# Kernel tuning notes

Measured on AMD Instinct MI355X. Metric: run time of the kernel, lower is better.

Reference implementation:

```python
import jax, jax.numpy as jnp
import numpy as np

DECAY = 0.99
EPS = 1e-05


def setup_inputs() -> dict:
    key = jax.random.key(0)
    k1, k2 = jax.random.split(key)
    B, C, H, W = 16, 64, 64, 64
    dim, n_embed = 64, 2048
    x = jax.random.normal(k1, (B, C, H, W), dtype=jnp.float32)
    embed = jax.random.normal(k2, (dim, n_embed), dtype=jnp.float32)
    cluster_size = jnp.zeros((n_embed,), dtype=jnp.float32)
    embed_avg = embed.copy()
    return {"x": x, "embed": embed, "cluster_size": cluster_size, "embed_avg": embed_avg}


def reference(x, embed, cluster_size, embed_avg):
    # x: [B, C, H, W], embed: [dim, n_embed]
    dim, n_embed = embed.shape
    xp = jnp.transpose(x, (0, 2, 3, 1))            # [B, H, W, dim]
    flat = xp.reshape(-1, dim)                     # [N, dim]

    # Pairwise squared distances: ||f||^2 - 2 f.E + ||e||^2  -> [N, n_embed]
    dist = (jnp.sum(flat * flat, axis=1, keepdims=True)
            - 2.0 * (flat @ embed)
            + jnp.sum(embed * embed, axis=0, keepdims=True))
    embed_ind_flat = jnp.argmin(dist, axis=1)      # [N]

    # Gather codes (embed_code)
    quantize = embed.T[embed_ind_flat].reshape(xp.shape)  # [B, H, W, dim]
    embed_ind = embed_ind_flat.reshape(xp.shape[:-1])     # [B, H, W]

    # Training-mode EMA codebook update (functional; buffers returned)
    counts = jax.ops.segment_sum(jnp.ones_like(embed_ind_flat, dtype=flat.dtype),
                                 embed_ind_flat, num_segments=n_embed)      # onehot.sum(0)
    embed_sum = jax.ops.segment_sum(flat, embed_ind_flat,
                                    num_segments=n_embed).T                 # flat.T @ onehot -> [dim, n_embed]
    new_cluster_size = DECAY * cluster_size + (1.0 - DECAY) * counts
    new_embed_avg = DECAY * embed_avg + (1.0 - DECAY) * embed_sum
    n = jnp.sum(new_cluster_size)
    cs = (new_cluster_size + EPS) / (n + n_embed * EPS) * n
    new_embed = new_embed_avg / cs[None, :]

    diff = jnp.mean((jax.lax.stop_gradient(quantize) - xp) ** 2)
    quantize_st = xp + jax.lax.stop_gradient(quantize - xp)
    out = jnp.transpose(quantize_st, (0, 3, 1, 2))  # back to NCHW
    return out, diff, embed_ind, new_embed, new_cluster_size, new_embed_avg
```

## Files before the change

kernel.cpp:

```cpp
#include <hip/hip_runtime.h>
#include <stdint.h>

#define DIM 64
#define NE 2048
#define NROWS 65536
#define HW 4096

#define DECAYF 0.99f
#define OMDF ((float)(1.0 - 0.99))
#define EPSF 1e-5f
#define NEPSF ((float)(2048.0 * 1e-5))

typedef _Float16 f16x8 __attribute__((ext_vector_type(8)));
typedef float f32x4 __attribute__((ext_vector_type(4)));

#define SPLIT_SCALE 1024.0f
#define SPLIT_INV 0.0009765625f

__global__ __launch_bounds__(256) void se_kernel(const float* __restrict__ E,
                                                 float* __restrict__ se) {
  int j = blockIdx.x * 256 + threadIdx.x;
  float s = 0.f;
#pragma unroll
  for (int d = 0; d < DIM; ++d) {
    float v = E[d * NE + j];
    s += v * v;
  }
  se[j] = s;
}

__global__ __launch_bounds__(256) void epack_kernel(const float* __restrict__ E,
                                                    _Float16* __restrict__ Eh,
                                                    _Float16* __restrict__ El) {
  int task = blockIdx.x * 256 + threadIdx.x;
  int l = task & 63;
  int ks = (task >> 6) & 1;
  int t = task >> 7;
  int j = t * 16 + (l & 15);
  int d0 = ks * 32 + ((l >> 4) & 3) * 8;
  _Float16 h8[8], l8[8];
#pragma unroll
  for (int r = 0; r < 8; ++r) {
    float v = E[(d0 + r) * NE + j];
    _Float16 h = (_Float16)v;
    h8[r] = h;
    l8[r] = (_Float16)((v - (float)h) * SPLIT_SCALE);
  }
  *(f16x8*)(Eh + (size_t)task * 8) = *(f16x8*)h8;
  *(f16x8*)(El + (size_t)task * 8) = *(f16x8*)l8;
}

#define MFMA16(A, B, C) __builtin_amdgcn_mfma_f32_16x16x32_f16(A, B, C, 0, 0, 0)

#define COMPUTE_TILE(T, B0, B1, B2, B3, SEJ)                              \
  {                                                                       \
    _Pragma("unroll") for (int rt = 0; rt < 4; ++rt) {                    \
      f32x4 a1 = {0.f, 0.f, 0.f, 0.f};                                    \
      f32x4 a2 = {0.f, 0.f, 0.f, 0.f};                                    \
      a1 = MFMA16(xh[rt][0], B0, a1);                                     \
      a1 = MFMA16(xh[rt][1], B1, a1);                                     \
      a2 = MFMA16(xh[rt][0], B2, a2);                                     \
      a2 = MFMA16(xh[rt][1], B3, a2);                                     \
      a2 = MFMA16(xl[rt][0], B0, a2);                                     \
      a2 = MFMA16(xl[rt][1], B1, a2);                                     \
      _Pragma("unroll") for (int q = 0; q < 4; ++q) {                     \
        float dot = fmaf(a2[q], SPLIT_INV, a1[q]);                        \
        float dist = fmaf(-2.f, dot, SEJ);                                \
        if (dist < bv[rt][q]) { bv[rt][q] = dist; bi[rt][q] = (T)*16 + lc; } \
      }                                                                   \
    }                                                                     \
  }

__global__ __launch_bounds__(256, 1) void argmin_mfma_kernel(
    const float* __restrict__ x, const _Float16* __restrict__ Eh,
    const _Float16* __restrict__ El, const float* __restrict__ se,
    int* __restrict__ ind, float* __restrict__ ind_f) {
  const int tid = threadIdx.x;
  const int lane = tid & 63;
  const int wv = tid >> 6;
  const int R0 = blockIdx.x * 256 + wv * 64;
  const int lg = (lane >> 4) & 3;
  const int lc = lane & 15;

  f16x8 xh[4][2], xl[4][2];
#pragma unroll
  for (int rt = 0; rt < 4; ++rt) {
#pragma unroll
    for (int ks = 0; ks < 2; ++ks) {
      int r_glob = R0 + rt * 16 + lc;
      const float* xr = x + (size_t)(r_glob >> 12) * (DIM * HW) + (r_glob & 4095);
      int d0 = ks * 32 + lg * 8;
      _Float16 h8[8], l8[8];
#pragma unroll
      for (int e = 0; e < 8; ++e) {
        float v = xr[(d0 + e) * HW];
        _Float16 h = (_Float16)v;
        h8[e] = h;
        l8[e] = (_Float16)((v - (float)h) * SPLIT_SCALE);
      }
      xh[rt][ks] = *(f16x8*)h8;
      xl[rt][ks] = *(f16x8*)l8;
    }
  }

  float bv[4][4];
  int bi[4][4];
#pragma unroll
  for (int rt = 0; rt < 4; ++rt)
#pragma unroll
    for (int q = 0; q < 4; ++q) { bv[rt][q] = 3.4e38f; bi[rt][q] = 0; }

  const size_t lo = (size_t)lane * 8;
  f16x8 c0 = *(const f16x8*)(Eh + lo);
  f16x8 c1 = *(const f16x8*)(Eh + 512 + lo);
  f16x8 c2 = *(const f16x8*)(El + lo);
  f16x8 c3 = *(const f16x8*)(El + 512 + lo);
  float seC = se[lc];

  for (int t = 0; t < NE / 16; t += 2) {
    f16x8 n0 = *(const f16x8*)(Eh + (size_t)(t + 1) * 1024 + lo);
    f16x8 n1 = *(const f16x8*)(Eh + (size_t)(t + 1) * 1024 + 512 + lo);
    f16x8 n2 = *(const f16x8*)(El + (size_t)(t + 1) * 1024 + lo);
    f16x8 n3 = *(const f16x8*)(El + (size_t)(t + 1) * 1024 + 512 + lo);
    float seN = se[(t + 1) * 16 + lc];

    COMPUTE_TILE(t, c0, c1, c2, c3, seC);

    if (t + 2 < NE / 16) {
      c0 = *(const f16x8*)(Eh + (size_t)(t + 2) * 1024 + lo);
      c1 = *(const f16x8*)(Eh + (size_t)(t + 2) * 1024 + 512 + lo);
      c2 = *(const f16x8*)(El + (size_t)(t + 2) * 1024 + lo);
      c3 = *(const f16x8*)(El + (size_t)(t + 2) * 1024 + 512 + lo);
      seC = se[(t + 2) * 16 + lc];
    }

    COMPUTE_TILE(t + 1, n0, n1, n2, n3, seN);
  }

#pragma unroll
  for (int rt = 0; rt < 4; ++rt) {
#pragma unroll
    for (int q = 0; q < 4; ++q) {
      float v = bv[rt][q];
      int ix = bi[rt][q];
#pragma unroll
      for (int off = 1; off < 16; off <<= 1) {
        float ov = __shfl_xor(v, off, 64);
        int oi = __shfl_xor(ix, off, 64);
        if (ov < v || (ov == v && oi < ix)) { v = ov; ix = oi; }
      }
      if (lc == 0) {
        int grow = R0 + rt * 16 + lg * 4 + q;
        ind[grow] = ix;
        ind_f[grow] = (float)ix;
      }
    }
  }
}

__global__ __launch_bounds__(256) void esum_fused_kernel(const float* __restrict__ x,
                                                         const float* __restrict__ E,
                                                         const int* __restrict__ ind,
                                                         float* __restrict__ out,
                                                         float* __restrict__ diff_acc,
                                                         float* __restrict__ pesum,
                                                         int* __restrict__ pcnt) {
  const int d = blockIdx.x >> 2;
  const int bg = blockIdx.x & 3;
  __shared__ float h[4][NE];
  __shared__ int cnt[NE];
  const int tid = threadIdx.x;
  const int w = tid >> 6;
  float* hf = &h[0][0];
#pragma unroll
  for (int u = 0; u < 32; ++u) hf[u * 256 + tid] = 0.f;
  if (d == 0) {
#pragma unroll
    for (int u = 0; u < 8; ++u) cnt[u * 256 + tid] = 0;
  }
  __syncthreads();
  const float* Ed = E + d * NE;
  float local = 0.f;
  for (int b = bg * 4; b < bg * 4 + 4; ++b) {
    const int* ib = ind + b * 4096;
    const float* xb = x + ((size_t)b * DIM + d) * 4096;
    float* ob = out + ((size_t)b * DIM + d) * 4096;
#pragma unroll 4
    for (int it = 0; it < 16; ++it) {
      int i = it * 256 + tid;
      int idx = ib[i];
      float xv = xb[i];
      float qv = Ed[idx];
      float dq = qv - xv;
      ob[i] = xv + dq;
      local += dq * dq;
      atomicAdd(&h[w][idx], xv);
      if (d == 0) atomicAdd(&cnt[idx], 1);
    }
  }
#pragma unroll
  for (int off = 32; off > 0; off >>= 1) local += __shfl_down(local, off, 64);
  __shared__ float wsum[4];
  if ((tid & 63) == 0) wsum[tid >> 6] = local;
  __syncthreads();
  if (tid == 0) {
    float s = (wsum[0] + wsum[1]) + (wsum[2] + wsum[3]);
    atomicAdd(diff_acc, s * (1.f / 4194304.f));
  }
  float* pe = pesum + ((size_t)bg * DIM + d) * NE;
#pragma unroll
  for (int u = 0; u < 8; ++u) {
    int j = u * 256 + tid;
    pe[j] = (h[0][j] + h[1][j]) + (h[2][j] + h[3][j]);
  }
  if (d == 0) {
    int* pc = pcnt + bg * NE;
#pragma unroll
    for (int u = 0; u < 8; ++u) {
      int j = u * 256 + tid;
      pc[j] = cnt[j];
    }
  }
}

__global__ __launch_bounds__(1024) void finalize_a4(const float* __restrict__ cs_in,
                                                    const int* __restrict__ pcnt,
                                                    float* __restrict__ ncs_slot,
                                                    float* __restrict__ n_out) {
  const int t = threadIdx.x;
  float local = 0.f;
#pragma unroll
  for (int u = 0; u < 2; ++u) {
    int k = u * 1024 + t;
    int c = (pcnt[k] + pcnt[NE + k]) + (pcnt[2 * NE + k] + pcnt[3 * NE + k]);
    float v = DECAYF * cs_in[k] + OMDF * (float)c;
    ncs_slot[k] = v;
    local += v;
  }
#pragma unroll
  for (int off = 32; off > 0; off >>= 1) local += __shfl_down(local, off, 64);
  __shared__ float red[16];
  if ((t & 63) == 0) red[t >> 6] = local;
  __syncthreads();
  if (t == 0) {
    float s = 0.f;
#pragma unroll
    for (int k = 0; k < 16; ++k) s += red[k];
    *n_out = s;
  }
}

__global__ __launch_bounds__(256) void finalize_b4(const float* __restrict__ ea_in,
                                                   const float* __restrict__ pesum,
                                                   const float* __restrict__ ncs_slot,
                                                   const float* __restrict__ n_out,
                                                   float* __restrict__ nea_slot,
                                                   float* __restrict__ ne_slot) {
  const int k = blockIdx.x * 256 + threadIdx.x;
  const float n = *n_out;
  const size_t P = (size_t)DIM * NE;
  float es = (pesum[k] + pesum[P + k]) + (pesum[2 * P + k] + pesum[3 * P + k]);
  float nea = DECAYF * ea_in[k] + OMDF * es;
  nea_slot[k] = nea;
  float ncs = ncs_slot[k & (NE - 1)];
  float cs = (ncs + EPSF) / (n + NEPSF) * n;
  ne_slot[k] = nea / cs;
}

#define BRF 128
#define TCF 128
#define NTF (NE / TCF)
__global__ __launch_bounds__(256, 2) void argmin_lds_kernel(const float* __restrict__ x,
                                                            const float* __restrict__ E,
                                                            const float* __restrict__ se,
                                                            int* __restrict__ ind,
                                                            float* __restrict__ ind_f) {
  __shared__ float Xs[DIM][BRF];
  __shared__ float Es[DIM][TCF];
  const int tid = threadIdx.x;
  const int rg = tid >> 4;
  const int cg = tid & 15;
  const int B0 = blockIdx.x * BRF;
  const float* xb = x + (size_t)(B0 >> 12) * (DIM * HW) + (B0 & 4095);
  float* Xf = &Xs[0][0];
#pragma unroll
  for (int k = 0; k < 8; ++k) {
    int i = k * 1024 + tid * 4;
    *(float4*)(Xf + i) = *(const float4*)(xb + (i >> 7) * HW + (i & 127));
  }
  float bv[8];
  int bi[8];
#pragma unroll
  for (int i2 = 0; i2 < 8; ++i2) { bv[i2] = 3.4e38f; bi[i2] = 0; }
  float* Ef = &Es[0][0];
  for (int t = 0; t < NTF; ++t) {
    __syncthreads();
#pragma unroll
    for (int k = 0; k < 8; ++k) {
      int i = k * 1024 + tid * 4;
      *(float4*)(Ef + i) = *(const float4*)(E + (i >> 7) * NE + t * TCF + (i & 127));
    }
    __syncthreads();
    float acc[8][8];
#pragma unroll
    for (int i2 = 0; i2 < 8; ++i2)
#pragma unroll
      for (int j = 0; j < 8; ++j) acc[i2][j] = 0.f;
#pragma unroll 8
    for (int d = 0; d < DIM; ++d) {
      float4 xa = *(const float4*)&Xs[d][rg * 8];
      float4 xc = *(const float4*)&Xs[d][rg * 8 + 4];
      float4 ea = *(const float4*)&Es[d][cg * 4];
      float4 ec = *(const float4*)&Es[d][cg * 4 + 64];
      float xr[8] = {xa.x, xa.y, xa.z, xa.w, xc.x, xc.y, xc.z, xc.w};
      float er[8] = {ea.x, ea.y, ea.z, ea.w, ec.x, ec.y, ec.z, ec.w};
#pragma unroll
      for (int i2 = 0; i2 < 8; ++i2)
#pragma unroll
        for (int j = 0; j < 8; ++j) acc[i2][j] = fmaf(xr[i2], er[j], acc[i2][j]);
    }
    float4 s0 = *(const float4*)(se + t * TCF + cg * 4);
    float4 s1 = *(const float4*)(se + t * TCF + cg * 4 + 64);
    float sv[8] = {s0.x, s0.y, s0.z, s0.w, s1.x, s1.y, s1.z, s1.w};
#pragma unroll
    for (int i2 = 0; i2 < 8; ++i2) {
#pragma unroll
      for (int j = 0; j < 8; ++j) {
        float dist = fmaf(-2.f, acc[i2][j], sv[j]);
        if (dist < bv[i2]) {
          bv[i2] = dist;
          bi[i2] = t * TCF + (j >> 2) * 64 + cg * 4 + (j & 3);
        }
      }
    }
  }
#pragma unroll
  for (int i2 = 0; i2 < 8; ++i2) {
    float v = bv[i2];
    int ix = bi[i2];
#pragma unroll
    for (int off = 1; off < 16; off <<= 1) {
      float ov = __shfl_xor(v, off, 64);
      int oi = __shfl_xor(ix, off, 64);
      if (ov < v || (ov == v && oi < ix)) { v = ov; ix = oi; }
    }
    bv[i2] = v;
    bi[i2] = ix;
  }
  if (cg == 0) {
#pragma unroll
    for (int i2 = 0; i2 < 8; ++i2) {
      int grow = B0 + rg * 8 + i2;
      ind[grow] = bi[i2];
      ind_f[grow] = (float)bi[i2];
    }
  }
}

__global__ __launch_bounds__(256) void outdiff_kernel(const float* __restrict__ x,
                                                      const float* __restrict__ E,
                                                      const int* __restrict__ ind,
                                                      float* __restrict__ out,
                                                      float* __restrict__ diff_acc) {
  const int t = threadIdx.x;
  float local = 0.f;
  const int base = blockIdx.x * 1024;
#pragma unroll
  for (int u = 0; u < 4; ++u) {
    int i = base + u * 256 + t;
    int hw = i & 4095;
    int bc = i >> 12;
    int c = bc & 63;
    int b = bc >> 6;
    int idx = ind[b * 4096 + hw];
    float xv = x[i];
    float qv = E[c * NE + idx];
    float dq = qv - xv;
    out[i] = xv + dq;
    local += dq * dq;
  }
#pragma unroll
  for (int off = 32; off > 0; off >>= 1) local += __shfl_down(local, off, 64);
  __shared__ float wsum[4];
  if ((t & 63) == 0) wsum[t >> 6] = local;
  __syncthreads();
  if (t == 0) {
    float s = wsum[0] + wsum[1] + wsum[2] + wsum[3];
    atomicAdd(diff_acc, s * (1.f / 4194304.f));
  }
}

__global__ __launch_bounds__(256) void scatter_atomic_kernel(const float* __restrict__ x,
                                                             const int* __restrict__ ind,
                                                             float* __restrict__ counts,
                                                             float* __restrict__ esum) {
  const int row = blockIdx.x * 256 + threadIdx.x;
  const int idx = ind[row];
  atomicAdd(&counts[idx], 1.f);
  const int b = row >> 12;
  const int hw = row & 4095;
  const float* xr = x + (size_t)b * (DIM * HW) + hw;
#pragma unroll
  for (int d = 0; d < DIM; ++d) atomicAdd(&esum[d * NE + idx], xr[d * HW]);
}

__global__ __launch_bounds__(1024) void finalize_a_float(const float* __restrict__ cs_in,
                                                         float* __restrict__ ncs_slot,
                                                         float* __restrict__ n_out) {
  const int t = threadIdx.x;
  float local = 0.f;
#pragma unroll
  for (int u = 0; u < 2; ++u) {
    int k = u * 1024 + t;
    float v = DECAYF * cs_in[k] + OMDF * ncs_slot[k];
    ncs_slot[k] = v;
    local += v;
  }
#pragma unroll
  for (int off = 32; off > 0; off >>= 1) local += __shfl_down(local, off, 64);
  __shared__ float red[16];
  if ((t & 63) == 0) red[t >> 6] = local;
  __syncthreads();
  if (t == 0) {
    float s = 0.f;
#pragma unroll
    for (int k = 0; k < 16; ++k) s += red[k];
    *n_out = s;
  }
}

__global__ __launch_bounds__(256) void finalize_b_inplace(const float* __restrict__ ea_in,
                                                          float* __restrict__ nea_slot,
                                                          const float* __restrict__ ncs_slot,
                                                          const float* __restrict__ n_out,
                                                          float* __restrict__ ne_slot) {
  const int k = blockIdx.x * 256 + threadIdx.x;
  const float n = *n_out;
  float nea = DECAYF * ea_in[k] + OMDF * nea_slot[k];
  nea_slot[k] = nea;
  float ncs = ncs_slot[k & (NE - 1)];
  float cs = (ncs + EPSF) / (n + NEPSF) * n;
  ne_slot[k] = nea / cs;
}

extern "C" void kernel_launch(void* const* d_in, const int* in_sizes, int n_in,
                              void* d_out, int out_size, void* d_ws, size_t ws_size,
                              hipStream_t stream) {
  const float* x = (const float*)d_in[0];
  const float* E = (const float*)d_in[1];
  const float* cs_in = (const float*)d_in[2];
  const float* ea_in = (const float*)d_in[3];
  float* out = (float*)d_out;

  const size_t O_OUT = 0;
  const size_t O_DIFF = 4194304;
  const size_t O_IND = 4194305;
  const size_t O_NE = 4259841;
  const size_t O_NCS = 4390913;
  const size_t O_NEA = 4392961;

  float* se = (float*)d_ws;
  int* ind = (int*)(se + NE);
  float* n_out = (float*)(ind + NROWS);
  int* pcnt = (int*)(n_out + 4);
  float* pesum = (float*)(pcnt + 4 * NE);
  _Float16* Ehpk = (_Float16*)pesum;
  _Float16* Elpk = Ehpk + (size_t)DIM * NE;
  const size_t need = (size_t)((char*)(pesum + 4 * (size_t)DIM * NE) - (char*)d_ws);
  const bool big_ws = ws_size >= need;

  hipMemsetAsync(out + O_DIFF, 0, 4, stream);
  se_kernel<<<NE / 256, 256, 0, stream>>>(E, se);

  if (big_ws) {
    epack_kernel<<<64, 256, 0, stream>>>(E, Ehpk, Elpk);
    argmin_mfma_kernel<<<NROWS / 256, 256, 0, stream>>>(x, Ehpk, Elpk, se, ind,
                                                        out + O_IND);
    esum_fused_kernel<<<DIM * 4, 256, 0, stream>>>(x, E, ind, out + O_OUT,
                                                   out + O_DIFF, pesum, pcnt);
    finalize_a4<<<1, 1024, 0, stream>>>(cs_in, pcnt, out + O_NCS, n_out);
    finalize_b4<<<DIM * NE / 256, 256, 0, stream>>>(ea_in, pesum, out + O_NCS, n_out,
                                                    out + O_NEA, out + O_NE);
  } else {
    argmin_lds_kernel<<<NROWS / BRF, 256, 0, stream>>>(x, E, se, ind, out + O_IND);
    outdiff_kernel<<<4096, 256, 0, stream>>>(x, E, ind, out + O_OUT, out + O_DIFF);
    hipMemsetAsync(out + O_NCS, 0, NE * 4, stream);
    hipMemsetAsync(out + O_NEA, 0, (size_t)DIM * NE * 4, stream);
    scatter_atomic_kernel<<<NROWS / 256, 256, 0, stream>>>(x, ind, out + O_NCS,
                                                           out + O_NEA);
    finalize_a_float<<<1, 1024, 0, stream>>>(cs_in, out + O_NCS, n_out);
    finalize_b_inplace<<<DIM * NE / 256, 256, 0, stream>>>(ea_in, out + O_NEA,
                                                           out + O_NCS, n_out,
                                                           out + O_NE);
  }
}
```

Measured before the change: 118.0 us.

## Split codebook scan across waves and merge argmin through shared memory

The argmin kernel now assigns 64 rows per block and has each of the four waves scan a quarter of the codebook, instead of each wave scanning the full codebook for its own rows. Partial minima are combined through shared memory after a barrier. This launches four times as many blocks to raise occupancy and latency hiding on the GPU. In exchange, each wave redundantly loads and splits the same x rows, and an extra LDS reduction and sync are added.

Measured after the change: 111.5 us. 5.5% less time.

```diff
diff --git a/kernel.cpp b/kernel.cpp
--- a/kernel.cpp
+++ b/kernel.cpp
@@ -78,7 +78,7 @@
   const int tid = threadIdx.x;
   const int lane = tid & 63;
   const int wv = tid >> 6;
-  const int R0 = blockIdx.x * 256 + wv * 64;
+  const int R0 = blockIdx.x * 64;
   const int lg = (lane >> 4) & 3;
   const int lc = lane & 15;
 
@@ -111,13 +111,14 @@
     for (int q = 0; q < 4; ++q) { bv[rt][q] = 3.4e38f; bi[rt][q] = 0; }
 
   const size_t lo = (size_t)lane * 8;
-  f16x8 c0 = *(const f16x8*)(Eh + lo);
-  f16x8 c1 = *(const f16x8*)(Eh + 512 + lo);
-  f16x8 c2 = *(const f16x8*)(El + lo);
-  f16x8 c3 = *(const f16x8*)(El + 512 + lo);
-  float seC = se[lc];
-
-  for (int t = 0; t < NE / 16; t += 2) {
+  const int t0 = wv * 32;
+  f16x8 c0 = *(const f16x8*)(Eh + (size_t)t0 * 1024 + lo);
+  f16x8 c1 = *(const f16x8*)(Eh + (size_t)t0 * 1024 + 512 + lo);
+  f16x8 c2 = *(const f16x8*)(El + (size_t)t0 * 1024 + lo);
+  f16x8 c3 = *(const f16x8*)(El + (size_t)t0 * 1024 + 512 + lo);
+  float seC = se[t0 * 16 + lc];
+
+  for (int t = t0; t < t0 + 32; t += 2) {
     f16x8 n0 = *(const f16x8*)(Eh + (size_t)(t + 1) * 1024 + lo);
     f16x8 n1 = *(const f16x8*)(Eh + (size_t)(t + 1) * 1024 + 512 + lo);
     f16x8 n2 = *(const f16x8*)(El + (size_t)(t + 1) * 1024 + lo);
@@ -126,7 +127,7 @@
 
     COMPUTE_TILE(t, c0, c1, c2, c3, seC);
 
-    if (t + 2 < NE / 16) {
+    if (t + 2 < t0 + 32) {
       c0 = *(const f16x8*)(Eh + (size_t)(t + 2) * 1024 + lo);
       c1 = *(const f16x8*)(Eh + (size_t)(t + 2) * 1024 + 512 + lo);
       c2 = *(const f16x8*)(El + (size_t)(t + 2) * 1024 + lo);
@@ -137,6 +138,8 @@
     COMPUTE_TILE(t + 1, n0, n1, n2, n3, seN);
   }
 
+  __shared__ float sv4[4][64];
+  __shared__ int si4[4][64];
 #pragma unroll
   for (int rt = 0; rt < 4; ++rt) {
 #pragma unroll
@@ -150,11 +153,24 @@
         if (ov < v || (ov == v && oi < ix)) { v = ov; ix = oi; }
       }
       if (lc == 0) {
-        int grow = R0 + rt * 16 + lg * 4 + q;
-        ind[grow] = ix;
-        ind_f[grow] = (float)ix;
+        int lrow = rt * 16 + lg * 4 + q;
+        sv4[wv][lrow] = v;
+        si4[wv][lrow] = ix;
       }
     }
+  }
+  __syncthreads();
+  if (tid < 64) {
+    float v = sv4[0][tid];
+    int ix = si4[0][tid];
+#pragma unroll
+    for (int w = 1; w < 4; ++w) {
+      float ov = sv4[w][tid];
+      int oi = si4[w][tid];
+      if (ov < v) { v = ov; ix = oi; }
+    }
+    ind[R0 + tid] = ix;
+    ind_f[R0 + tid] = (float)ix;
   }
 }
 
@@ -474,8 +490,8 @@
 
   if (big_ws) {
     epack_kernel<<<64, 256, 0, stream>>>(E, Ehpk, Elpk);
-    argmin_mfma_kernel<<<NROWS / 256, 256, 0, stream>>>(x, Ehpk, Elpk, se, ind,
-                                                        out + O_IND);
+    argmin_mfma_kernel<<<NROWS / 64, 256, 0, stream>>>(x, Ehpk, Elpk, se, ind,
+                                                       out + O_IND);
     esum_fused_kernel<<<DIM * 4, 256, 0, stream>>>(x, E, ind, out + O_OUT,
                                                    out + O_DIFF, pesum, pcnt);
     finalize_a4<<<1, 1024, 0, stream>>>(cs_in, pcnt, out + O_NCS, n_out);
```
